# Performance work log

Measured on AMD Instinct MI355X. Metric: run time of the kernel, lower is better.

## Reference

```python
import jax, jax.numpy as jnp
import numpy as np

BETA = 0.95
NUM_STEPS = 32


def setup_inputs() -> dict:
    key = jax.random.key(0)
    ks = jax.random.split(key, 6)
    B, IN, D, P = 1024, 512, 256, 8
    total = D * P
    x = jax.random.normal(ks[0], (B, IN), jnp.float32)
    W_proj = jax.random.normal(ks[1], (IN, total), jnp.float32) / np.sqrt(IN)
    b_proj = jnp.zeros((total,), jnp.float32)
    # uniform threshold distribution, sorted: linspace(0.5, 2.0, P)
    thresholds = jnp.linspace(0.5, 2.0, P, dtype=jnp.float32)
    rate_W = jax.random.normal(ks[2], (P, 1), jnp.float32) / np.sqrt(P)
    rate_b = jnp.zeros((1,), jnp.float32)
    conv1_w = jax.random.normal(ks[3], (P // 2, P, 3), jnp.float32) / np.sqrt(P * 3)
    conv1_b = jnp.zeros((P // 2,), jnp.float32)
    conv2_w = jax.random.normal(ks[4], (1, P // 2, 1), jnp.float32) / np.sqrt(P // 2)
    conv2_b = jnp.zeros((1,), jnp.float32)
    fusion = jnp.array([0.6, 0.4], jnp.float32)
    return dict(x=x, W_proj=W_proj, b_proj=b_proj, thresholds=thresholds,
                rate_W=rate_W, rate_b=rate_b, conv1_w=conv1_w, conv1_b=conv1_b,
                conv2_w=conv2_w, conv2_b=conv2_b, fusion=fusion)


def _conv1d(x, w, b):
    # x: [N, C_in, T], w: [C_out, C_in, K] -> [N, C_out, T] (SAME padding)
    y = jax.lax.conv_general_dilated(x, w, window_strides=(1,), padding='SAME',
                                     dimension_numbers=('NCH', 'OIH', 'NCH'))
    return y + b[None, :, None]


def reference(x, W_proj, b_proj, thresholds, rate_W, rate_b,
              conv1_w, conv1_b, conv2_w, conv2_b, fusion):
    B = x.shape[0]
    P = thresholds.shape[0]
    D = W_proj.shape[1] // P
    # constant input current per neuron: [B, D, P]
    I = (x @ W_proj + b_proj).reshape(B, D, P)

    # LIF recurrence (snntorch Leaky, reset_mechanism='subtract'):
    #   reset = H(mem_prev - thr); mem = beta*mem_prev + I - reset*thr; spk = H(mem - thr)
    def step(mem, _):
        reset = (mem > thresholds).astype(mem.dtype)
        mem = BETA * mem + I - reset * thresholds
        spk = (mem > thresholds).astype(mem.dtype)
        return mem, spk

    mem0 = jnp.zeros((B, D, P), x.dtype)
    _, spikes = jax.lax.scan(step, mem0, None, length=NUM_STEPS)  # [T, B, D, P]

    # rate branch
    rates = spikes.mean(axis=0)                        # [B, D, P]
    rate_dec = (rates @ rate_W)[..., 0] + rate_b[0]    # [B, D]

    # temporal branch: [B*D, P, T]
    s = jnp.transpose(spikes, (1, 2, 3, 0)).reshape(B * D, P, NUM_STEPS)
    h = jax.nn.relu(_conv1d(s, conv1_w, conv1_b))
    h = _conv1d(h, conv2_w, conv2_b)                   # [B*D, 1, T]
    temp_dec = h.mean(axis=-1).reshape(B, D)

    fw = jax.nn.softmax(fusion)
    return fw[0] * rate_dec + fw[1] * temp_dec
```

## Files before the change

kernel.cpp:

```cpp
#include <hip/hip_runtime.h>
#include <type_traits>


constexpr int IN_DIM  = 512;
constexpr int D_DIM   = 256;
constexpr int NTOT    = 2048;
constexpr int T_STEPS = 32;

typedef _Float16 f16x8 __attribute__((ext_vector_type(8)));
typedef float    f32x4 __attribute__((ext_vector_type(4)));
typedef ushort   ushort8 __attribute__((ext_vector_type(8)));

#define GLOBAL_AS __attribute__((address_space(1)))
#define LDS_AS    __attribute__((address_space(3)))

__device__ __forceinline__ void split_f16(float v, ushort& h, ushort& l) {
    const _Float16 hf = (_Float16)v;
    const _Float16 lf = (_Float16)((v - (float)hf) * 2048.0f);
    h = __builtin_bit_cast(ushort, hf);
    l = __builtin_bit_cast(ushort, lf);
}

__global__ __launch_bounds__(256)
void popcode_prep(const float* __restrict__ x, const float* __restrict__ Wp,
                  ushort* __restrict__ Ah, ushort* __restrict__ Al,
                  ushort* __restrict__ Bh, ushort* __restrict__ Bl)
{
    __shared__ float tile[64][68];
    const int t = threadIdx.x;
    if (blockIdx.x < 256) {
        const int idx = (blockIdx.x * 256 + t) * 8;
        float v[8];
        *reinterpret_cast<float4*>(v)     = *reinterpret_cast<const float4*>(x + idx);
        *reinterpret_cast<float4*>(v + 4) = *reinterpret_cast<const float4*>(x + idx + 4);
        __align__(16) ushort h[8], l[8];
#pragma unroll
        for (int j = 0; j < 8; ++j) split_f16(v[j], h[j], l[j]);
        *reinterpret_cast<ushort8*>(Ah + idx) = *reinterpret_cast<const ushort8*>(h);
        *reinterpret_cast<ushort8*>(Al + idx) = *reinterpret_cast<const ushort8*>(l);
    } else {
        const int ib = blockIdx.x - 256;
        const int k0 = (ib >> 5) * 64;
        const int c0 = (ib & 31) * 64;
        {
            const int r = t >> 2, cq = (t & 3) * 16;
#pragma unroll
            for (int j = 0; j < 4; ++j)
                *reinterpret_cast<float4*>(&tile[r][cq + j * 4]) =
                    *reinterpret_cast<const float4*>(Wp + (size_t)(k0 + r) * NTOT + c0 + cq + j * 4);
        }
        __syncthreads();
        const int c = t & 63, kq = (t >> 6) * 16;
        __align__(16) ushort h[16], l[16];
#pragma unroll
        for (int j = 0; j < 16; ++j) split_f16(tile[kq + j][c], h[j], l[j]);
        ushort* dh = Bh + (size_t)(c0 + c) * 512 + k0 + kq;
        ushort* dl = Bl + (size_t)(c0 + c) * 512 + k0 + kq;
        *reinterpret_cast<ushort8*>(dh)     = *reinterpret_cast<const ushort8*>(h);
        *reinterpret_cast<ushort8*>(dh + 8) = *reinterpret_cast<const ushort8*>(h + 8);
        *reinterpret_cast<ushort8*>(dl)     = *reinterpret_cast<const ushort8*>(l);
        *reinterpret_cast<ushort8*>(dl + 8) = *reinterpret_cast<const ushort8*>(l + 8);
    }
}

__global__ __launch_bounds__(256, 2)
void popcode_mfma(const ushort* __restrict__ Ah_g, const ushort* __restrict__ Al_g,
                  const ushort* __restrict__ Bh_g, const ushort* __restrict__ Bl_g,
                  float* __restrict__ Iout)
{
    __shared__ __align__(16) ushort Lds[2][4][64][32];

    const int tid  = threadIdx.x;
    const int w    = tid >> 6;
    const int lane = tid & 63;

    const int wg = (blockIdx.x & 7) * 64 + (blockIdx.x >> 3);
    const int b0 = (wg & 15) * 64;
    const int c0 = (wg >> 4) * 64;

    const ushort* gbase = (w == 0) ? Ah_g : (w == 1) ? Al_g : (w == 2) ? Bh_g : Bl_g;
    const int     t0    = (w < 2) ? b0 : c0;
    const int     srow  = lane >> 2;
    const int     schk  = (lane & 3) * 8;

    const int wr = (w >> 1) * 32;
    const int wc = (w & 1) * 32;
    const int lr = lane & 15;
    const int lg = lane >> 4;

    const f32x4 zero = {0.f, 0.f, 0.f, 0.f};
    f32x4 acch[2][2] = {{zero, zero}, {zero, zero}};
    f32x4 accl[2][2] = {{zero, zero}, {zero, zero}};

    LDS_AS char* lds0 = (LDS_AS char*)&Lds[0][0][0][0];

    auto stage = [&](int buf, int kt) {
        const int koff = kt * 32 + schk;
#pragma unroll
        for (int i = 0; i < 4; ++i) {
            const ushort* src = gbase + (size_t)(t0 + srow + 16 * i) * 512 + koff;
            const int loff = __builtin_amdgcn_readfirstlane(buf * 16384 + w * 4096 + i * 1024);
            __builtin_amdgcn_global_load_lds((const GLOBAL_AS uint*)src,
                                             (LDS_AS uint*)(lds0 + loff), 16, 0, 0);
        }
    };

    auto compute = [&](int buf) {
        f16x8 ah[2], al[2], bh[2], bl[2];
#pragma unroll
        for (int m = 0; m < 2; ++m) {
            const int row = wr + m * 16 + lr;
            ah[m] = *(const f16x8*)&Lds[buf][0][row][lg * 8];
            al[m] = *(const f16x8*)&Lds[buf][1][row][lg * 8];
        }
#pragma unroll
        for (int n = 0; n < 2; ++n) {
            const int col = wc + n * 16 + lr;
            bh[n] = *(const f16x8*)&Lds[buf][2][col][lg * 8];
            bl[n] = *(const f16x8*)&Lds[buf][3][col][lg * 8];
        }
#pragma unroll
        for (int m = 0; m < 2; ++m)
#pragma unroll
            for (int n = 0; n < 2; ++n) {
                acch[m][n] = __builtin_amdgcn_mfma_f32_16x16x32_f16(ah[m], bh[n], acch[m][n], 0, 0, 0);
                accl[m][n] = __builtin_amdgcn_mfma_f32_16x16x32_f16(al[m], bh[n], accl[m][n], 0, 0, 0);
                accl[m][n] = __builtin_amdgcn_mfma_f32_16x16x32_f16(ah[m], bl[n], accl[m][n], 0, 0, 0);
            }
    };

    stage(0, 0);
    __syncthreads();
    for (int kt = 0; kt < 16; ++kt) {
        if (kt < 15) stage((kt + 1) & 1, kt + 1);
        compute(kt & 1);
        __syncthreads();
    }

    const float s = 1.0f / 2048.0f;
#pragma unroll
    for (int m = 0; m < 2; ++m)
#pragma unroll
        for (int n = 0; n < 2; ++n) {
            float* dst = Iout + (size_t)(b0 + wr + m * 16 + lg * 4) * NTOT
                              + c0 + wc + n * 16 + lr;
#pragma unroll
            for (int v = 0; v < 4; ++v)
                dst[(size_t)v * NTOT] = acch[m][n][v] + accl[m][n][v] * s;
        }
}

__global__ __launch_bounds__(256)
void popcode_epi(const float* __restrict__ Iin,
                 const float* __restrict__ bp,
                 const float* __restrict__ thrs,
                 const float* __restrict__ rateW,
                 const float* __restrict__ rateB,
                 const float* __restrict__ c1w,
                 const float* __restrict__ c1b,
                 const float* __restrict__ c2w,
                 const float* __restrict__ c2b,
                 const float* __restrict__ fus,
                 float* __restrict__ out)
{
    __shared__ float lut[3][2][16][4];
    __shared__ float wlds[96];
    __shared__ uint4 exch[256];

    const int tid = threadIdx.x;
    const int wv  = tid >> 6;
    const int h   = wv & 1;
    const int nl  = ((wv >> 1) << 6) | (tid & 63);
    const int n   = blockIdx.x * 128 + nl;
    const int b   = n >> 8;
    const int d   = n & 255;

    if (tid < 96) wlds[tid] = c1w[tid];
    __syncthreads();
    for (int e = tid; e < 384; e += 256) {
        const int k  = e >> 7;
        const int j  = (e >> 6) & 1;
        const int nb = (e >> 2) & 15;
        const int c  = e & 3;
        float v = (k == 1 && j == 0) ? c1b[c] : 0.f;
#pragma unroll
        for (int p = 0; p < 4; ++p)
            v = fmaf((float)((nb >> p) & 1), wlds[(c * 8 + j * 4 + p) * 3 + k], v);
        (&lut[0][0][0][0])[e] = v;
    }

    float w2c[4];
#pragma unroll
    for (int c = 0; c < 4; ++c) w2c[c] = c2w[c];
    float rW[4];
#pragma unroll
    for (int p = 0; p < 4; ++p) rW[p] = rateW[h * 4 + p];
    const float rb_ = rateB[0];
    const float bb2 = c2b[0];
    const float f0 = fus[0], f1 = fus[1];
    const float fm = fmaxf(f0, f1);
    const float e0 = __expf(f0 - fm), e1 = __expf(f1 - fm);
    const float inv = 1.f / (e0 + e1);
    const float fw0 = e0 * inv, fw1 = e1 * inv;

    const size_t base = (size_t)b * NTOT + d * 8 + h * 4;
    const float4 iv   = *reinterpret_cast<const float4*>(Iin + base);
    const float4 bpv  = *reinterpret_cast<const float4*>(bp + d * 8 + h * 4);
    const float4 tv   = *reinterpret_cast<const float4*>(thrs + h * 4);
    float Iv[4]  = {iv.x + bpv.x, iv.y + bpv.y, iv.z + bpv.z, iv.w + bpv.w};
    float thr[4] = {tv.x, tv.y, tv.z, tv.w};
    float Imt[4], mem[4];
    bool  spk[4];
#pragma unroll
    for (int p = 0; p < 4; ++p) {
        Imt[p] = Iv[p] - thr[p];
        mem[p] = 0.f;
        spk[p] = false;
    }

    unsigned nib[4] = {0u, 0u, 0u, 0u};
#pragma unroll
    for (int t = 0; t < T_STEPS; ++t) {
        unsigned nb = 0u;
#pragma unroll
        for (int p = 0; p < 4; ++p) {
            mem[p] = 0.95f * mem[p] + (spk[p] ? Imt[p] : Iv[p]);
            spk[p] = mem[p] > thr[p];
            nb |= spk[p] ? (1u << p) : 0u;
        }
        nib[t >> 3] |= nb << (4 * (t & 7));
    }

    float rsum = 0.f;
#pragma unroll
    for (int p = 0; p < 4; ++p) {
        const unsigned m = 0x11111111u << p;
        const int cnt = __popc(nib[0] & m) + __popc(nib[1] & m)
                      + __popc(nib[2] & m) + __popc(nib[3] & m);
        rsum = fmaf((float)cnt, rW[p], rsum);
    }

    __syncthreads();
    exch[tid] = uint4{nib[0], nib[1], nib[2], nib[3]};
    __syncthreads();
    const uint4 pr = exch[tid ^ 64];
    const unsigned prn[4] = {pr.x, pr.y, pr.z, pr.w};
    unsigned lo[4], hi[4];
#pragma unroll
    for (int w = 0; w < 4; ++w) {
        lo[w] = h ? prn[w] : nib[w];
        hi[w] = h ? nib[w] : prn[w];
    }

    auto getn = [&](int t, const unsigned* a) -> unsigned {
        return (a[t >> 3] >> (4 * (t & 7))) & 15u;
    };
    const float* lutf = &lut[0][0][0][0];
    float tacc = 0.f;

    auto conv_half = [&](auto T0C) {
        constexpr int T0 = T0C.value;
        unsigned nlp = (T0 == 0) ? 0u : getn(T0 - 1, lo);
        unsigned nhp = (T0 == 0) ? 0u : getn(T0 - 1, hi);
        unsigned nlc = getn(T0, lo);
        unsigned nhc = getn(T0, hi);
#pragma unroll
        for (int i = 0; i < 16; ++i) {
            const int t = T0 + i;
            const unsigned nln = (t < 31) ? getn(t + 1, lo) : 0u;
            const unsigned nhn = (t < 31) ? getn(t + 1, hi) : 0u;
            const float4 a0 = *reinterpret_cast<const float4*>(lutf + (nlp     ) * 4);
            const float4 a1 = *reinterpret_cast<const float4*>(lutf + (nhp + 16) * 4);
            const float4 b0 = *reinterpret_cast<const float4*>(lutf + (nlc + 32) * 4);
            const float4 b1 = *reinterpret_cast<const float4*>(lutf + (nhc + 48) * 4);
            const float4 c0 = *reinterpret_cast<const float4*>(lutf + (nln + 64) * 4);
            const float4 c1 = *reinterpret_cast<const float4*>(lutf + (nhn + 80) * 4);
            const float h0_ = ((a0.x + a1.x) + (b0.x + b1.x)) + (c0.x + c1.x);
            const float h1_ = ((a0.y + a1.y) + (b0.y + b1.y)) + (c0.y + c1.y);
            const float h2_ = ((a0.z + a1.z) + (b0.z + b1.z)) + (c0.z + c1.z);
            const float h3_ = ((a0.w + a1.w) + (b0.w + b1.w)) + (c0.w + c1.w);
            tacc = fmaf(fmaxf(h0_, 0.f), w2c[0], tacc);
            tacc = fmaf(fmaxf(h1_, 0.f), w2c[1], tacc);
            tacc = fmaf(fmaxf(h2_, 0.f), w2c[2], tacc);
            tacc = fmaf(fmaxf(h3_, 0.f), w2c[3], tacc);
            nlp = nlc; nhp = nhc; nlc = nln; nhc = nhn;
        }
    };
    if (h == 0) conv_half(std::integral_constant<int, 0>{});
    else        conv_half(std::integral_constant<int, 16>{});

    __syncthreads();
    float2* e2 = reinterpret_cast<float2*>(exch);
    e2[tid] = float2{rsum, tacc};
    __syncthreads();
    const float2 q = e2[tid ^ 64];
    rsum += q.x;
    tacc += q.y;

    if (h == 0) {
        const float rdec = rsum * (1.f / 32.f) + rb_;
        const float temp = tacc * (1.f / 32.f) + bb2;
        out[b * D_DIM + d] = fw0 * rdec + fw1 * temp;
    }
}

extern "C" void kernel_launch(void* const* d_in, const int* in_sizes, int n_in,
                              void* d_out, int out_size, void* d_ws, size_t ws_size,
                              hipStream_t stream) {
    const float* x     = (const float*)d_in[0];
    const float* Wp    = (const float*)d_in[1];
    const float* bp    = (const float*)d_in[2];
    const float* thrs  = (const float*)d_in[3];
    const float* rateW = (const float*)d_in[4];
    const float* rateB = (const float*)d_in[5];
    const float* c1w   = (const float*)d_in[6];
    const float* c1b   = (const float*)d_in[7];
    const float* c2w   = (const float*)d_in[8];
    const float* c2b   = (const float*)d_in[9];
    const float* fus   = (const float*)d_in[10];
    float* out = (float*)d_out;
    float* ws  = (float*)d_ws;

    ushort* Ah = reinterpret_cast<ushort*>(ws);
    ushort* Al = Ah + 1024 * 512;
    ushort* Bh = Al + 1024 * 512;
    ushort* Bl = Bh + 2048 * 512;
    float*  I  = ws + 1536 * 1024;

    popcode_prep<<<dim3(512), dim3(256), 0, stream>>>(x, Wp, Ah, Al, Bh, Bl);
    popcode_mfma<<<dim3(512), dim3(256), 0, stream>>>(Ah, Al, Bh, Bl, I);
    popcode_epi<<<dim3(2048), dim3(256), 0, stream>>>(
        I, bp, thrs, rateW, rateB, c1w, c1b, c2w, c2b, fus, out);
}
```

Measured before the change: 110.1 us.

## Fuse GEMM with LIF/conv epilogue and fix prep transpose bank conflicts

The MFMA GEMM kernel and the spiking epilogue kernel are merged: each block writes its 64x64 current tile into LDS and then runs the LIF recurrence, rate decode and temporal conv for its 512 (batch,D) neurons directly. This removes the 8 MB global round-trip of the current matrix and one kernel launch. Each thread now handles all 8 populations for one neuron over two passes, so the cross-wave exchange is no longer needed. In return the epilogue parallelism falls from 2048x256 threads to 512x256 threads, LDS use per block grows, and register pressure rises. The prep transpose also gets a padded LDS tile and a new thread mapping to cut bank conflicts.

```diff
diff --git a/kernel.cpp b/kernel.cpp
--- a/kernel.cpp
+++ b/kernel.cpp
@@ -1,5 +1,4 @@
 #include <hip/hip_runtime.h>
-#include <type_traits>
 
 
 constexpr int IN_DIM  = 512;
@@ -26,7 +25,7 @@
                   ushort* __restrict__ Ah, ushort* __restrict__ Al,
                   ushort* __restrict__ Bh, ushort* __restrict__ Bl)
 {
-    __shared__ float tile[64][68];
+    __shared__ float tile[64][69];
     const int t = threadIdx.x;
     if (blockIdx.x < 256) {
         const int idx = (blockIdx.x * 256 + t) * 8;
@@ -50,12 +49,12 @@
                     *reinterpret_cast<const float4*>(Wp + (size_t)(k0 + r) * NTOT + c0 + cq + j * 4);
         }
         __syncthreads();
-        const int c = t & 63, kq = (t >> 6) * 16;
+        const int rr = t >> 2, kc2 = (t & 3) * 16;
         __align__(16) ushort h[16], l[16];
 #pragma unroll
-        for (int j = 0; j < 16; ++j) split_f16(tile[kq + j][c], h[j], l[j]);
-        ushort* dh = Bh + (size_t)(c0 + c) * 512 + k0 + kq;
-        ushort* dl = Bl + (size_t)(c0 + c) * 512 + k0 + kq;
+        for (int j = 0; j < 16; ++j) split_f16(tile[kc2 + j][rr], h[j], l[j]);
+        ushort* dh = Bh + (size_t)(c0 + rr) * 512 + k0 + kc2;
+        ushort* dl = Bl + (size_t)(c0 + rr) * 512 + k0 + kc2;
         *reinterpret_cast<ushort8*>(dh)     = *reinterpret_cast<const ushort8*>(h);
         *reinterpret_cast<ushort8*>(dh + 8) = *reinterpret_cast<const ushort8*>(h + 8);
         *reinterpret_cast<ushort8*>(dl)     = *reinterpret_cast<const ushort8*>(l);
@@ -64,11 +63,23 @@
 }
 
 __global__ __launch_bounds__(256, 2)
-void popcode_mfma(const ushort* __restrict__ Ah_g, const ushort* __restrict__ Al_g,
-                  const ushort* __restrict__ Bh_g, const ushort* __restrict__ Bl_g,
-                  float* __restrict__ Iout)
+void popcode_fused(const ushort* __restrict__ Ah_g, const ushort* __restrict__ Al_g,
+                   const ushort* __restrict__ Bh_g, const ushort* __restrict__ Bl_g,
+                   const float* __restrict__ bp,
+                   const float* __restrict__ thrs,
+                   const float* __restrict__ rateW,
+                   const float* __restrict__ rateB,
+                   const float* __restrict__ c1w,
+                   const float* __restrict__ c1b,
+                   const float* __restrict__ c2w,
+                   const float* __restrict__ c2b,
+                   const float* __restrict__ fus,
+                   float* __restrict__ out)
 {
     __shared__ __align__(16) ushort Lds[2][4][64][32];
+    __shared__ float Itile[64][65];
+    __shared__ float lut[3][2][16][4];
+    __shared__ float wlds[96];
 
     const int tid  = threadIdx.x;
     const int w    = tid >> 6;
@@ -129,54 +140,10 @@
             }
     };
 
+    if (tid < 96) wlds[tid] = c1w[tid];
     stage(0, 0);
     __syncthreads();
-    for (int kt = 0; kt < 16; ++kt) {
-        if (kt < 15) stage((kt + 1) & 1, kt + 1);
-        compute(kt & 1);
-        __syncthreads();
-    }
-
-    const float s = 1.0f / 2048.0f;
-#pragma unroll
-    for (int m = 0; m < 2; ++m)
-#pragma unroll
-        for (int n = 0; n < 2; ++n) {
-            float* dst = Iout + (size_t)(b0 + wr + m * 16 + lg * 4) * NTOT
-                              + c0 + wc + n * 16 + lr;
-#pragma unroll
-            for (int v = 0; v < 4; ++v)
-                dst[(size_t)v * NTOT] = acch[m][n][v] + accl[m][n][v] * s;
-        }
-}
-
-__global__ __launch_bounds__(256)
-void popcode_epi(const float* __restrict__ Iin,
-                 const float* __restrict__ bp,
-                 const float* __restrict__ thrs,
-                 const float* __restrict__ rateW,
-                 const float* __restrict__ rateB,
-                 const float* __restrict__ c1w,
-                 const float* __restrict__ c1b,
-                 const float* __restrict__ c2w,
-                 const float* __restrict__ c2b,
-                 const float* __restrict__ fus,
-                 float* __restrict__ out)
-{
-    __shared__ float lut[3][2][16][4];
-    __shared__ float wlds[96];
-    __shared__ uint4 exch[256];
-
-    const int tid = threadIdx.x;
-    const int wv  = tid >> 6;
-    const int h   = wv & 1;
-    const int nl  = ((wv >> 1) << 6) | (tid & 63);
-    const int n   = blockIdx.x * 128 + nl;
-    const int b   = n >> 8;
-    const int d   = n & 255;
-
-    if (tid < 96) wlds[tid] = c1w[tid];
-    __syncthreads();
+
     for (int e = tid; e < 384; e += 256) {
         const int k  = e >> 7;
         const int j  = (e >> 6) & 1;
@@ -189,12 +156,29 @@
         (&lut[0][0][0][0])[e] = v;
     }
 
+    for (int kt = 0; kt < 16; ++kt) {
+        if (kt < 15) stage((kt + 1) & 1, kt + 1);
+        compute(kt & 1);
+        __syncthreads();
+    }
+
+    const float s = 1.0f / 2048.0f;
+#pragma unroll
+    for (int m = 0; m < 2; ++m)
+#pragma unroll
+        for (int n = 0; n < 2; ++n)
+#pragma unroll
+            for (int v = 0; v < 4; ++v)
+                Itile[wr + m * 16 + lg * 4 + v][wc + n * 16 + lr] =
+                    acch[m][n][v] + accl[m][n][v] * s;
+    __syncthreads();
+
     float w2c[4];
 #pragma unroll
     for (int c = 0; c < 4; ++c) w2c[c] = c2w[c];
-    float rW[4];
-#pragma unroll
-    for (int p = 0; p < 4; ++p) rW[p] = rateW[h * 4 + p];
+    float rW[8], thrv[8];
+#pragma unroll
+    for (int p = 0; p < 8; ++p) { rW[p] = rateW[p]; thrv[p] = thrs[p]; }
     const float rb_ = rateB[0];
     const float bb2 = c2b[0];
     const float f0 = fus[0], f1 = fus[1];
@@ -203,104 +187,88 @@
     const float inv = 1.f / (e0 + e1);
     const float fw0 = e0 * inv, fw1 = e1 * inv;
 
-    const size_t base = (size_t)b * NTOT + d * 8 + h * 4;
-    const float4 iv   = *reinterpret_cast<const float4*>(Iin + base);
-    const float4 bpv  = *reinterpret_cast<const float4*>(bp + d * 8 + h * 4);
-    const float4 tv   = *reinterpret_cast<const float4*>(thrs + h * 4);
-    float Iv[4]  = {iv.x + bpv.x, iv.y + bpv.y, iv.z + bpv.z, iv.w + bpv.w};
-    float thr[4] = {tv.x, tv.y, tv.z, tv.w};
-    float Imt[4], mem[4];
-    bool  spk[4];
-#pragma unroll
-    for (int p = 0; p < 4; ++p) {
-        Imt[p] = Iv[p] - thr[p];
-        mem[p] = 0.f;
-        spk[p] = false;
-    }
-
-    unsigned nib[4] = {0u, 0u, 0u, 0u};
-#pragma unroll
-    for (int t = 0; t < T_STEPS; ++t) {
-        unsigned nb = 0u;
+    const float* lutf = &lut[0][0][0][0];
+
+    for (int half = 0; half < 2; ++half) {
+        const int nb   = tid + half * 256;
+        const int row  = nb >> 3;
+        const int dloc = nb & 7;
+        const int dg   = (c0 >> 3) + dloc;
+
+        const float* ip = &Itile[row][dloc * 8];
+        const float4 bv0 = *reinterpret_cast<const float4*>(bp + dg * 8);
+        const float4 bv1 = *reinterpret_cast<const float4*>(bp + dg * 8 + 4);
+        const float bpx[8] = {bv0.x, bv0.y, bv0.z, bv0.w, bv1.x, bv1.y, bv1.z, bv1.w};
+
+        float Iv[8], Imt[8], mem[8];
+        bool  spk[8];
+#pragma unroll
+        for (int p = 0; p < 8; ++p) {
+            Iv[p]  = ip[p] + bpx[p];
+            Imt[p] = Iv[p] - thrv[p];
+            mem[p] = 0.f;
+            spk[p] = false;
+        }
+
+        unsigned nibL[4] = {0u, 0u, 0u, 0u}, nibH[4] = {0u, 0u, 0u, 0u};
+#pragma unroll
+        for (int t = 0; t < T_STEPS; ++t) {
+            unsigned bl_ = 0u, bh_ = 0u;
+#pragma unroll
+            for (int p = 0; p < 8; ++p) {
+                mem[p] = 0.95f * mem[p] + (spk[p] ? Imt[p] : Iv[p]);
+                spk[p] = mem[p] > thrv[p];
+            }
+#pragma unroll
+            for (int p = 0; p < 4; ++p) bl_ |= spk[p] ? (1u << p) : 0u;
+#pragma unroll
+            for (int p = 4; p < 8; ++p) bh_ |= spk[p] ? (1u << (p - 4)) : 0u;
+            nibL[t >> 3] |= bl_ << (4 * (t & 7));
+            nibH[t >> 3] |= bh_ << (4 * (t & 7));
+        }
+
+        float rsum = 0.f;
 #pragma unroll
         for (int p = 0; p < 4; ++p) {
-            mem[p] = 0.95f * mem[p] + (spk[p] ? Imt[p] : Iv[p]);
-            spk[p] = mem[p] > thr[p];
-            nb |= spk[p] ? (1u << p) : 0u;
-        }
-        nib[t >> 3] |= nb << (4 * (t & 7));
-    }
-
-    float rsum = 0.f;
-#pragma unroll
-    for (int p = 0; p < 4; ++p) {
-        const unsigned m = 0x11111111u << p;
-        const int cnt = __popc(nib[0] & m) + __popc(nib[1] & m)
-                      + __popc(nib[2] & m) + __popc(nib[3] & m);
-        rsum = fmaf((float)cnt, rW[p], rsum);
-    }
-
-    __syncthreads();
-    exch[tid] = uint4{nib[0], nib[1], nib[2], nib[3]};
-    __syncthreads();
-    const uint4 pr = exch[tid ^ 64];
-    const unsigned prn[4] = {pr.x, pr.y, pr.z, pr.w};
-    unsigned lo[4], hi[4];
-#pragma unroll
-    for (int w = 0; w < 4; ++w) {
-        lo[w] = h ? prn[w] : nib[w];
-        hi[w] = h ? nib[w] : prn[w];
-    }
-
-    auto getn = [&](int t, const unsigned* a) -> unsigned {
-        return (a[t >> 3] >> (4 * (t & 7))) & 15u;
-    };
-    const float* lutf = &lut[0][0][0][0];
-    float tacc = 0.f;
-
-    auto conv_half = [&](auto T0C) {
-        constexpr int T0 = T0C.value;
-        unsigned nlp = (T0 == 0) ? 0u : getn(T0 - 1, lo);
-        unsigned nhp = (T0 == 0) ? 0u : getn(T0 - 1, hi);
-        unsigned nlc = getn(T0, lo);
-        unsigned nhc = getn(T0, hi);
-#pragma unroll
-        for (int i = 0; i < 16; ++i) {
-            const int t = T0 + i;
-            const unsigned nln = (t < 31) ? getn(t + 1, lo) : 0u;
-            const unsigned nhn = (t < 31) ? getn(t + 1, hi) : 0u;
+            const unsigned m = 0x11111111u << p;
+            const int cL = __popc(nibL[0] & m) + __popc(nibL[1] & m)
+                         + __popc(nibL[2] & m) + __popc(nibL[3] & m);
+            const int cH = __popc(nibH[0] & m) + __popc(nibH[1] & m)
+                         + __popc(nibH[2] & m) + __popc(nibH[3] & m);
+            rsum = fmaf((float)cL, rW[p], rsum);
+            rsum = fmaf((float)cH, rW[4 + p], rsum);
+        }
+
+        auto getn = [](const unsigned* a, int t) -> unsigned {
+            return (a[t >> 3] >> (4 * (t & 7))) & 15u;
+        };
+        float tacc = 0.f;
+        unsigned nlp = 0u, nhp = 0u;
+        unsigned nlc = getn(nibL, 0), nhc = getn(nibH, 0);
+#pragma unroll
+        for (int t = 0; t < T_STEPS; ++t) {
+            const unsigned nln = (t < 31) ? getn(nibL, t + 1) : 0u;
+            const unsigned nhn = (t < 31) ? getn(nibH, t + 1) : 0u;
             const float4 a0 = *reinterpret_cast<const float4*>(lutf + (nlp     ) * 4);
             const float4 a1 = *reinterpret_cast<const float4*>(lutf + (nhp + 16) * 4);
             const float4 b0 = *reinterpret_cast<const float4*>(lutf + (nlc + 32) * 4);
             const float4 b1 = *reinterpret_cast<const float4*>(lutf + (nhc + 48) * 4);
-            const float4 c0 = *reinterpret_cast<const float4*>(lutf + (nln + 64) * 4);
-            const float4 c1 = *reinterpret_cast<const float4*>(lutf + (nhn + 80) * 4);
-            const float h0_ = ((a0.x + a1.x) + (b0.x + b1.x)) + (c0.x + c1.x);
-            const float h1_ = ((a0.y + a1.y) + (b0.y + b1.y)) + (c0.y + c1.y);
-            const float h2_ = ((a0.z + a1.z) + (b0.z + b1.z)) + (c0.z + c1.z);
-            const float h3_ = ((a0.w + a1.w) + (b0.w + b1.w)) + (c0.w + c1.w);
+            const float4 c0v = *reinterpret_cast<const float4*>(lutf + (nln + 64) * 4);
+            const float4 c1v = *reinterpret_cast<const float4*>(lutf + (nhn + 80) * 4);
+            const float h0_ = ((a0.x + a1.x) + (b0.x + b1.x)) + (c0v.x + c1v.x);
+            const float h1_ = ((a0.y + a1.y) + (b0.y + b1.y)) + (c0v.y + c1v.y);
+            const float h2_ = ((a0.z + a1.z) + (b0.z + b1.z)) + (c0v.z + c1v.z);
+            const float h3_ = ((a0.w + a1.w) + (b0.w + b1.w)) + (c0v.w + c1v.w);
             tacc = fmaf(fmaxf(h0_, 0.f), w2c[0], tacc);
             tacc = fmaf(fmaxf(h1_, 0.f), w2c[1], tacc);
             tacc = fmaf(fmaxf(h2_, 0.f), w2c[2], tacc);
             tacc = fmaf(fmaxf(h3_, 0.f), w2c[3], tacc);
             nlp = nlc; nhp = nhc; nlc = nln; nhc = nhn;
         }
-    };
-    if (h == 0) conv_half(std::integral_constant<int, 0>{});
-    else        conv_half(std::integral_constant<int, 16>{});
-
-    __syncthreads();
-    float2* e2 = reinterpret_cast<float2*>(exch);
-    e2[tid] = float2{rsum, tacc};
-    __syncthreads();
-    const float2 q = e2[tid ^ 64];
-    rsum += q.x;
-    tacc += q.y;
-
-    if (h == 0) {
+
         const float rdec = rsum * (1.f / 32.f) + rb_;
         const float temp = tacc * (1.f / 32.f) + bb2;
-        out[b * D_DIM + d] = fw0 * rdec + fw1 * temp;
+        out[(b0 + row) * D_DIM + dg] = fw0 * rdec + fw1 * temp;
     }
 }
 
@@ -325,10 +293,8 @@
     ushort* Al = Ah + 1024 * 512;
     ushort* Bh = Al + 1024 * 512;
     ushort* Bl = Bh + 2048 * 512;
-    float*  I  = ws + 1536 * 1024;
 
     popcode_prep<<<dim3(512), dim3(256), 0, stream>>>(x, Wp, Ah, Al, Bh, Bl);
-    popcode_mfma<<<dim3(512), dim3(256), 0, stream>>>(Ah, Al, Bh, Bl, I);
-    popcode_epi<<<dim3(2048), dim3(256), 0, stream>>>(
-        I, bp, thrs, rateW, rateB, c1w, c1b, c2w, c2b, fus, out);
+    popcode_fused<<<dim3(512), dim3(256), 0, stream>>>(
+        Ah, Al, Bh, Bl, bp, thrs, rateW, rateB, c1w, c1b, c2w, c2b, fus, out);
 }
```

Result: faster. 106.3 us, median of 2 (-3.4%).
